# Optimization experiments

Hardware: AMD Instinct MI355X
Metric: run time of the kernel (lower is better)

The kernel has to match this reference:

```python
import jax, jax.numpy as jnp
import numpy as np

B, C, T = 8, 1024, 1024
H, K, R = 8, 8, 8
DQK = C // K      # 128, per-head q/k channels
DFC1 = C // R     # 128, FC hidden
DINNER = C // H   # 128, per-head FC output


def setup_inputs() -> dict:
    key = jax.random.key(0)
    ks = jax.random.split(key, 12)
    s_in = 1.0 / np.sqrt(C)
    s_fc = 1.0 / np.sqrt(DFC1)
    return {
        "x": jax.random.normal(ks[0], (B, C, T), dtype=jnp.float32),
        # per-head 1x1 conv weights stacked over heads
        "Wq": jax.random.normal(ks[1], (H, DQK, C), dtype=jnp.float32) * s_in,
        "bq": jax.random.normal(ks[2], (H, DQK), dtype=jnp.float32) * 0.01,
        "Wk": jax.random.normal(ks[3], (H, DQK, C), dtype=jnp.float32) * s_in,
        "bk": jax.random.normal(ks[4], (H, DQK), dtype=jnp.float32) * 0.01,
        "Wv": jax.random.normal(ks[5], (H, C, C), dtype=jnp.float32) * s_in,
        "bv": jax.random.normal(ks[6], (H, C), dtype=jnp.float32) * 0.01,
        # gamma is zero-init in torch; use small random values to exercise the math
        "gamma": jax.random.normal(ks[7], (H,), dtype=jnp.float32) * 0.1,
        # post-concat MLP (nn.Linear weights, shape (out, in))
        "W1": jax.random.normal(ks[8], (DFC1, C), dtype=jnp.float32) * s_in,
        "b1": jax.random.normal(ks[9], (DFC1,), dtype=jnp.float32) * 0.01,
        "W2": jax.random.normal(ks[10], (DINNER, DFC1), dtype=jnp.float32) * s_fc,
        "b2": jax.random.normal(ks[11], (DINNER,), dtype=jnp.float32) * 0.01,
    }


def reference(x, Wq, bq, Wk, bk, Wv, bv, gamma, W1, b1, W2, b2):
    # x: (B, C, T). 1x1 Conv1d == channel-wise linear; batch all H heads at once.
    q = jnp.einsum('hoc,bct->bhot', Wq, x) + bq[None, :, :, None]  # (B,H,DQK,T)
    k = jnp.einsum('hoc,bct->bhot', Wk, x) + bk[None, :, :, None]  # (B,H,DQK,T)
    v = jnp.einsum('hoc,bct->bhot', Wv, x) + bv[None, :, :, None]  # (B,H,C,T)
    # energy[b,h,t,s] = q[:, :, :, t] . k[:, :, :, s]; softmax over s (no scaling, as in source)
    attn = jax.nn.softmax(jnp.einsum('bhot,bhos->bhts', q, k), axis=-1)  # (B,H,T,T)
    # out[b,h,c,t] = sum_s v[b,h,c,s] * attn[b,h,t,s]
    o = jnp.einsum('bhcs,bhts->bhct', v, attn)                     # (B,H,C,T)
    heads = gamma[None, :, None, None] * o + x[:, None, :, :]      # (B,H,C,T)
    # torch.stack(outs, 2): (B, C, H, T)
    out = heads.transpose(0, 2, 1, 3).reshape(B, C, H * T)
    out = out.transpose(0, 2, 1)                                   # (B, H*T, C)
    # fcs: Linear -> ReLU -> Dropout(eval: identity) -> Linear -> ReLU -> Dropout
    out = jax.nn.relu(out @ W1.T + b1)
    out = jax.nn.relu(out @ W2.T + b2)                             # (B, H*T, DINNER)
    out = out.transpose(0, 2, 1).reshape(B, DINNER * H, T)         # (B, C, T)
    return out + x
```

## Files before the change

kernel.cpp:

```cpp
#include <hip/hip_runtime.h>
#include <hip/hip_bf16.h>

typedef __hip_bfloat16 bf16;
typedef __attribute__((ext_vector_type(8))) __bf16 bf16x8;
typedef __attribute__((ext_vector_type(4))) float f32x4;

typedef const __attribute__((address_space(1))) void gvoid;
typedef __attribute__((address_space(3))) void lvoid;

template<int MODE, int QKLAY>
__global__ __launch_bounds__(256, 2)
void gemm256(const bf16* __restrict__ A, long lda, long sAb, long sAh,
             const bf16* __restrict__ B, long ldb, long sBb, long sBh,
             void* __restrict__ Cv, long ldc, long sCb, long sCh,
             int K,
             const float* __restrict__ bias, long sBiasZ,
             const float* __restrict__ gamma,
             const bf16* __restrict__ xt, long ldxt)
{
    __shared__ bf16 ring[3][(256 + 128) * 32];
    const int nt4 = QKLAY ? blockIdx.x : (blockIdx.x >> 3);
    const int zh  = QKLAY ? 0 : (blockIdx.x & 7);
    const int zb  = QKLAY ? 0 : blockIdx.z;
    const bf16* Ab = A + (long)zb * sAb + (long)zh * sAh + (long)blockIdx.y * 256 * lda;
    const bf16* Bb = B + (long)zb * sBb + (long)zh * sBh + (long)nt4 * 128 * ldb;
    const int tid = threadIdx.x;
    const int wave = tid >> 6, lane = tid & 63;
    const int col = lane & 15, quad = lane >> 4;
    const int wm = wave * 64;

    const bf16* aAddr[4];
    const bf16* bAddr[2];
    int aDst[4], bDst[2];
    #pragma unroll
    for (int i = 0; i < 4; ++i) {
        int cbase = i * 256 + wave * 64;
        int c = cbase + lane;
        int p = c >> 3;
        int sp = (c & 7) ^ (p & 7);
        int m = 2 * p + (sp >> 2);
        int j = sp & 3;
        aAddr[i] = Ab + (long)m * lda + (j << 3);
        aDst[i] = cbase * 8;
    }
    #pragma unroll
    for (int i = 0; i < 2; ++i) {
        int cbase = i * 256 + wave * 64;
        int c = cbase + lane;
        int p = c >> 3;
        int sp = (c & 7) ^ (p & 7);
        int m = 2 * p + (sp >> 2);
        int j = sp & 3;
        bAddr[i] = Bb + (long)m * ldb + (j << 3);
        bDst[i] = 8192 + cbase * 8;
    }

    int offA[4], offB[8];
    #pragma unroll
    for (int mi = 0; mi < 4; ++mi) {
        int m = wm + mi * 16 + col;
        int p = m >> 1;
        int s = (quad | ((m & 1) << 2)) ^ (p & 7);
        offA[mi] = p * 64 + s * 8;
    }
    #pragma unroll
    for (int ni = 0; ni < 8; ++ni) {
        int n = ni * 16 + col;
        int pn = n >> 1;
        int sn = (quad | ((n & 1) << 2)) ^ (pn & 7);
        offB[ni] = 8192 + pn * 64 + sn * 8;
    }

    f32x4 acc[4][8] = {};

    auto STAGE = [&](int rb) {
        bf16* base = &ring[rb][0];
        #pragma unroll
        for (int i = 0; i < 4; ++i) {
            __builtin_amdgcn_global_load_lds((gvoid*)aAddr[i], (lvoid*)(base + aDst[i]), 16, 0, 0);
            aAddr[i] += 32;
        }
        #pragma unroll
        for (int i = 0; i < 2; ++i) {
            __builtin_amdgcn_global_load_lds((gvoid*)bAddr[i], (lvoid*)(base + bDst[i]), 16, 0, 0);
            bAddr[i] += 32;
        }
    };

    const int NT = K >> 5;
    STAGE(0);
    STAGE(1);
    asm volatile("s_waitcnt vmcnt(6)" ::: "memory");
    __builtin_amdgcn_s_barrier();
    __builtin_amdgcn_sched_barrier(0);

    int rc = 0;
    for (int t = 0; t < NT; ++t) {
        int r2 = rc + 2; if (r2 >= 3) r2 -= 3;
        if (t + 2 < NT) STAGE(r2);
        const bf16* buf = &ring[rc][0];
        bf16x8 af[4], bfr[8];
        #pragma unroll
        for (int mi = 0; mi < 4; ++mi)
            af[mi] = *(const bf16x8*)(buf + offA[mi]);
        #pragma unroll
        for (int ni = 0; ni < 8; ++ni)
            bfr[ni] = *(const bf16x8*)(buf + offB[ni]);
        #pragma unroll
        for (int mi = 0; mi < 4; ++mi)
            #pragma unroll
            for (int ni = 0; ni < 8; ++ni)
                acc[mi][ni] = __builtin_amdgcn_mfma_f32_16x16x32_bf16(
                    af[mi], bfr[ni], acc[mi][ni], 0, 0, 0);
        if (t + 2 < NT)
            asm volatile("s_waitcnt vmcnt(6)" ::: "memory");
        else if (t + 1 < NT)
            asm volatile("s_waitcnt vmcnt(0)" ::: "memory");
        if (t + 1 < NT) {
            __builtin_amdgcn_s_barrier();
            __builtin_amdgcn_sched_barrier(0);
        }
        rc = rc + 1; if (rc >= 3) rc -= 3;
    }

    const long m0 = (long)blockIdx.y * 256 + wm;
    const long n0 = (long)nt4 * 128;
    float g = 0.f;
    if (MODE == 3) g = gamma[zh];
    float bn[8];
    if constexpr (MODE == 1) {
        #pragma unroll
        for (int ni = 0; ni < 8; ++ni)
            bn[ni] = bias[n0 + ni * 16 + col];
    }
    #pragma unroll
    for (int mi = 0; mi < 4; ++mi) {
        #pragma unroll
        for (int ni = 0; ni < 8; ++ni) {
            long mb = m0 + mi * 16 + quad * 4;
            long n  = n0 + ni * 16 + col;
            if constexpr (MODE == 0) {
                bf16* cp = (bf16*)Cv + (long)zb * sCb + (long)zh * sCh + mb * ldc + n;
                const float* bp = bias + zh * sBiasZ + mb;
                #pragma unroll
                for (int r = 0; r < 4; ++r) {
                    *cp = __float2bfloat16(acc[mi][ni][r] + bp[r]);
                    cp += ldc;
                }
            } else if constexpr (MODE == 1) {
                bf16* cp = (bf16*)Cv + mb * ldc + n;
                #pragma unroll
                for (int r = 0; r < 4; ++r) {
                    *cp = __float2bfloat16(acc[mi][ni][r] + bn[ni]);
                    cp += ldc;
                }
            } else {
                bf16* cp = (bf16*)Cv + (long)zb * sCb + (long)zh * sCh + mb * ldc + n;
                const bf16* xp = xt + (long)zb * 1048576 + mb * ldxt + n;
                #pragma unroll
                for (int r = 0; r < 4; ++r) {
                    float xv = __bfloat162float(*xp);
                    *cp = __float2bfloat16(g * acc[mi][ni][r] + xv);
                    cp += ldc;
                    xp += ldxt;
                }
            }
        }
    }
}

__global__ __launch_bounds__(256, 2)
void fc_fused(const bf16* __restrict__ ot,
              const bf16* __restrict__ W1b,
              const bf16* __restrict__ W2b,
              const float* __restrict__ b1,
              const float* __restrict__ b2,
              float* __restrict__ outp,
              const float* __restrict__ xf)
{
    __shared__ bf16 As[128 * 64];
    __shared__ bf16 Bs[128 * 64];
    __shared__ bf16 y1[128 * 128];
    const int tid = threadIdx.x;
    const int wave = tid >> 6, lane = tid & 63;
    const int col = lane & 15, quad = lane >> 4;
    const int wm = (wave & 1) * 64, wn = (wave >> 1) * 64;
    const bf16* Ab = ot + (long)blockIdx.y * 128 * 1024;

    const bf16* aAddr[4];
    const bf16* bAddr[4];
    #pragma unroll
    for (int i = 0; i < 4; ++i) {
        int cbase = i * 256 + wave * 64;
        int c = cbase + lane;
        int m = c >> 3, j = c & 7;
        int kch = ((j ^ (m & 7)) << 3);
        aAddr[i] = Ab + (long)m * 1024 + kch;
        bAddr[i] = W1b + (long)m * 1024 + kch;
    }
    int offA[2][4], offB[2][4];
    #pragma unroll
    for (int x = 0; x < 2; ++x) {
        int kq = x * 4 + quad;
        #pragma unroll
        for (int mi = 0; mi < 4; ++mi) {
            int m = wm + mi * 16 + col;
            offA[x][mi] = m * 64 + ((kq ^ (m & 7)) << 3);
            int n = wn + mi * 16 + col;
            offB[x][mi] = n * 64 + ((kq ^ (n & 7)) << 3);
        }
    }

    f32x4 acc[4][4] = {};
    for (int k0 = 0; k0 < 1024; k0 += 64) {
        __syncthreads();
        #pragma unroll
        for (int i = 0; i < 4; ++i) {
            int cbase = i * 256 + wave * 64;
            __builtin_amdgcn_global_load_lds(
                (gvoid*)aAddr[i], (lvoid*)(As + cbase * 8), 16, 0, 0);
            __builtin_amdgcn_global_load_lds(
                (gvoid*)bAddr[i], (lvoid*)(Bs + cbase * 8), 16, 0, 0);
            aAddr[i] += 64;
            bAddr[i] += 64;
        }
        __syncthreads();
        #pragma unroll
        for (int x = 0; x < 2; ++x) {
            bf16x8 af[4], bfr[4];
            #pragma unroll
            for (int mi = 0; mi < 4; ++mi)
                af[mi] = *(const bf16x8*)(As + offA[x][mi]);
            #pragma unroll
            for (int ni = 0; ni < 4; ++ni)
                bfr[ni] = *(const bf16x8*)(Bs + offB[x][ni]);
            #pragma unroll
            for (int mi = 0; mi < 4; ++mi)
                #pragma unroll
                for (int ni = 0; ni < 4; ++ni)
                    acc[mi][ni] = __builtin_amdgcn_mfma_f32_16x16x32_bf16(
                        af[mi], bfr[ni], acc[mi][ni], 0, 0, 0);
        }
    }

    float bn1[4];
    #pragma unroll
    for (int ni = 0; ni < 4; ++ni) bn1[ni] = b1[wn + ni * 16 + col];
    #pragma unroll
    for (int mi = 0; mi < 4; ++mi) {
        #pragma unroll
        for (int ni = 0; ni < 4; ++ni) {
            int mb = wm + mi * 16 + quad * 4;
            int n  = wn + ni * 16 + col;
            int nc = n >> 3, nr = n & 7;
            #pragma unroll
            for (int r = 0; r < 4; ++r) {
                float v = acc[mi][ni][r] + bn1[ni];
                v = v > 0.f ? v : 0.f;
                int m = mb + r;
                y1[m * 128 + (((nc) ^ (m & 7)) << 3) + nr] = __float2bfloat16(v);
            }
        }
    }
    __syncthreads();

    f32x4 acc2[4][4] = {};
    #pragma unroll
    for (int kk = 0; kk < 4; ++kk) {
        int kq = kk * 4 + quad;
        bf16x8 af2[4], bf2[4];
        #pragma unroll
        for (int mi = 0; mi < 4; ++mi) {
            int m = wm + mi * 16 + col;
            af2[mi] = *(const bf16x8*)(y1 + m * 128 + ((kq ^ (m & 7)) << 3));
        }
        #pragma unroll
        for (int ni = 0; ni < 4; ++ni) {
            int n = wn + ni * 16 + col;
            bf2[ni] = *(const bf16x8*)(W2b + n * 128 + kq * 8);
        }
        #pragma unroll
        for (int mi = 0; mi < 4; ++mi)
            #pragma unroll
            for (int ni = 0; ni < 4; ++ni)
                acc2[mi][ni] = __builtin_amdgcn_mfma_f32_16x16x32_bf16(
                    af2[mi], bf2[ni], acc2[mi][ni], 0, 0, 0);
    }

    float bn2[4];
    #pragma unroll
    for (int ni = 0; ni < 4; ++ni) bn2[ni] = b2[wn + ni * 16 + col];
    const long m0 = (long)blockIdx.y * 128 + wm;
    #pragma unroll
    for (int mi = 0; mi < 4; ++mi) {
        #pragma unroll
        for (int ni = 0; ni < 4; ++ni) {
            long mb = m0 + mi * 16 + quad * 4;
            long n  = wn + ni * 16 + col;
            #pragma unroll
            for (int r = 0; r < 4; ++r) {
                long m = mb + r;
                float v = acc2[mi][ni][r] + bn2[ni];
                v = v > 0.f ? v : 0.f;
                long bb = m >> 13, h = (m >> 10) & 7, t = m & 1023;
                long oi = bb * 1048576 + (n * 8 + h) * 1024 + t;
                outp[oi] = v + xf[oi];
            }
        }
    }
}

__global__ __launch_bounds__(256, 2)
void attn_fused(const bf16* __restrict__ qk, bf16* __restrict__ attn)
{
    constexpr int PAD = 1032;
    __shared__ __align__(16) char smraw[73728];
    __shared__ float red[2][4][32];
    bf16* Qs = (bf16*)smraw;
    bf16* Sbuf = (bf16*)smraw;

    const int z = blockIdx.x;
    const int zb = z >> 3, zh = z & 7;
    const int t0 = blockIdx.y * 32;
    const int tid = threadIdx.x, w = tid >> 6, lane = tid & 63;
    const int col = lane & 15, quad = lane >> 4;

    const bf16* Qbase = qk + ((long)zb * 1024 + t0) * 2048 + zh * 256;
    const bf16* Kbase = qk + (long)zb * 1024 * 2048 + zh * 256 + 128;

    auto stageK = [&](int slot, int si) {
        bf16* Ks = (bf16*)(smraw + 8192 + slot * 32768);
        const bf16* Kb = Kbase + (long)si * 128 * 2048;
        #pragma unroll
        for (int i = 0; i < 8; ++i) {
            int cbase = i * 256 + w * 64;
            int c = cbase + lane;
            int m = c >> 4, j = c & 15;
            __builtin_amdgcn_global_load_lds(
                (gvoid*)(Kb + (long)m * 2048 + ((j ^ (m & 7)) << 3)),
                (lvoid*)(Ks + cbase * 8), 16, 0, 0);
        }
    };

    #pragma unroll
    for (int i = 0; i < 2; ++i) {
        int cbase = i * 256 + w * 64;
        int c = cbase + lane;
        int m = c >> 4, j = c & 15;
        __builtin_amdgcn_global_load_lds(
            (gvoid*)(Qbase + (long)m * 2048 + ((j ^ (m & 7)) << 3)),
            (lvoid*)(Qs + cbase * 8), 16, 0, 0);
    }
    stageK(0, 0);
    stageK(1, 1);
    asm volatile("s_waitcnt vmcnt(8)" ::: "memory");
    __builtin_amdgcn_s_barrier();
    __builtin_amdgcn_sched_barrier(0);

    bf16x8 af[2][4];
    #pragma unroll
    for (int mi = 0; mi < 2; ++mi) {
        int m = mi * 16 + col;
        #pragma unroll
        for (int ki = 0; ki < 4; ++ki)
            af[mi][ki] = *(const bf16x8*)(Qs + m * 128 + ((((ki << 2) + quad) ^ (m & 7)) << 3));
    }

    f32x4 acc[2][16] = {};
    #pragma unroll
    for (int si = 0; si < 8; ++si) {
        const bf16* Ks = (const bf16*)(smraw + 8192 + (si & 1) * 32768);
        bf16x8 bfr[2][4];
        #pragma unroll
        for (int ni = 0; ni < 2; ++ni) {
            int n = w * 32 + ni * 16 + col;
            #pragma unroll
            for (int ki = 0; ki < 4; ++ki)
                bfr[ni][ki] = *(const bf16x8*)(Ks + n * 128 + ((((ki << 2) + quad) ^ (n & 7)) << 3));
        }
        asm volatile("s_waitcnt lgkmcnt(0)" ::: "memory");
        __builtin_amdgcn_sched_barrier(0);
        #pragma unroll
        for (int ki = 0; ki < 4; ++ki)
            #pragma unroll
            for (int mi = 0; mi < 2; ++mi)
                #pragma unroll
                for (int ni = 0; ni < 2; ++ni)
                    acc[mi][si * 2 + ni] = __builtin_amdgcn_mfma_f32_16x16x32_bf16(
                        af[mi][ki], bfr[ni][ki], acc[mi][si * 2 + ni], 0, 0, 0);
        __builtin_amdgcn_s_barrier();
        if (si + 2 < 8) {
            stageK(si & 1, si + 2);
            asm volatile("s_waitcnt vmcnt(8)" ::: "memory");
        } else {
            asm volatile("s_waitcnt vmcnt(0)" ::: "memory");
        }
        __builtin_amdgcn_s_barrier();
        __builtin_amdgcn_sched_barrier(0);
    }

    float rmx[2][4], rinv[2][4];
    #pragma unroll
    for (int mi = 0; mi < 2; ++mi)
        #pragma unroll
        for (int r = 0; r < 4; ++r) {
            float mx = acc[mi][0][r];
            #pragma unroll
            for (int j = 1; j < 16; ++j) mx = fmaxf(mx, acc[mi][j][r]);
            #pragma unroll
            for (int off = 1; off < 16; off <<= 1) mx = fmaxf(mx, __shfl_xor(mx, off, 64));
            rmx[mi][r] = mx;
        }
    if (col == 0) {
        #pragma unroll
        for (int mi = 0; mi < 2; ++mi)
            #pragma unroll
            for (int r = 0; r < 4; ++r)
                red[0][w][mi * 16 + quad * 4 + r] = rmx[mi][r];
    }
    __syncthreads();
    #pragma unroll
    for (int mi = 0; mi < 2; ++mi)
        #pragma unroll
        for (int r = 0; r < 4; ++r) {
            int row = mi * 16 + quad * 4 + r;
            rmx[mi][r] = fmaxf(fmaxf(red[0][0][row], red[0][1][row]),
                               fmaxf(red[0][2][row], red[0][3][row]));
        }
    #pragma unroll
    for (int mi = 0; mi < 2; ++mi)
        #pragma unroll
        for (int r = 0; r < 4; ++r) {
            float s = 0.f;
            #pragma unroll
            for (int j = 0; j < 16; ++j) {
                acc[mi][j][r] = __expf(acc[mi][j][r] - rmx[mi][r]);
                s += acc[mi][j][r];
            }
            #pragma unroll
            for (int off = 1; off < 16; off <<= 1) s += __shfl_xor(s, off, 64);
            rinv[mi][r] = s;
        }
    if (col == 0) {
        #pragma unroll
        for (int mi = 0; mi < 2; ++mi)
            #pragma unroll
            for (int r = 0; r < 4; ++r)
                red[1][w][mi * 16 + quad * 4 + r] = rinv[mi][r];
    }
    __syncthreads();
    #pragma unroll
    for (int mi = 0; mi < 2; ++mi)
        #pragma unroll
        for (int r = 0; r < 4; ++r) {
            int row = mi * 16 + quad * 4 + r;
            float s4 = red[1][0][row] + red[1][1][row] + red[1][2][row] + red[1][3][row];
            rinv[mi][r] = 1.0f / s4;
        }

    bf16* dst = attn + ((long)(zb * 8 + zh)) * 1048576 + (long)t0 * 1024;
    #pragma unroll
    for (int mi = 0; mi < 2; ++mi) {
        __syncthreads();
        #pragma unroll
        for (int j = 0; j < 16; ++j) {
            int colb = (j >> 1) * 128 + w * 32 + (j & 1) * 16 + col;
            #pragma unroll
            for (int r = 0; r < 4; ++r) {
                int rowh = quad * 4 + r;
                Sbuf[rowh * PAD + colb] = __float2bfloat16(acc[mi][j][r] * rinv[mi][r]);
            }
        }
        __syncthreads();
        #pragma unroll
        for (int i = 0; i < 8; ++i) {
            int c = i * 256 + tid;
            int rowh = c >> 7, jj = c & 127;
            bf16x8 vv = *(const bf16x8*)(Sbuf + rowh * PAD + jj * 8);
            *(bf16x8*)(dst + (long)(mi * 16 + rowh) * 1024 + jj * 8) = vv;
        }
    }
}

__global__ __launch_bounds__(256)
void transpose_cast_x(const float* __restrict__ x, bf16* __restrict__ xt)
{
    __shared__ float tile[32][33];
    int b = blockIdx.z;
    int c0 = blockIdx.y * 32, t0 = blockIdx.x * 32;
    int tx = threadIdx.x & 31, ty = threadIdx.x >> 5;
    const float* xb = x + (long)b * 1024 * 1024;
    #pragma unroll
    for (int i = 0; i < 4; ++i) {
        int c = ty + i * 8;
        tile[c][tx] = xb[(long)(c0 + c) * 1024 + t0 + tx];
    }
    __syncthreads();
    bf16* xtb = xt + (long)b * 1024 * 1024;
    #pragma unroll
    for (int i = 0; i < 4; ++i) {
        int t = ty + i * 8;
        xtb[(long)(t0 + t) * 1024 + c0 + tx] = __float2bfloat16(tile[tx][t]);
    }
}

__global__ __launch_bounds__(256)
void cast_f2b(const float* __restrict__ in, bf16* __restrict__ out, long n)
{
    long i = (long)blockIdx.x * 256 + threadIdx.x;
    long stride = (long)gridDim.x * 256;
    for (; i < n; i += stride) out[i] = __float2bfloat16(in[i]);
}

__global__ __launch_bounds__(256)
void build_wqk(const float* __restrict__ Wq, const float* __restrict__ Wk,
               const float* __restrict__ bq, const float* __restrict__ bk,
               bf16* __restrict__ Wqk, float* __restrict__ biasqk)
{
    long i = (long)blockIdx.x * 256 + threadIdx.x;
    long r = i >> 10, c = i & 1023;
    long h = r >> 8, rr = r & 255;
    float v = (rr < 128) ? Wq[(h * 128 + rr) * 1024 + c]
                         : Wk[(h * 128 + (rr - 128)) * 1024 + c];
    Wqk[i] = __float2bfloat16(v);
    if (c == 0)
        biasqk[r] = (rr < 128) ? bq[h * 128 + rr] : bk[h * 128 + rr - 128];
}

extern "C" void kernel_launch(void* const* d_in, const int* in_sizes, int n_in,
                              void* d_out, int out_size, void* d_ws, size_t ws_size,
                              hipStream_t stream)
{
    const float* x     = (const float*)d_in[0];
    const float* Wq    = (const float*)d_in[1];
    const float* bq    = (const float*)d_in[2];
    const float* Wk    = (const float*)d_in[3];
    const float* bk    = (const float*)d_in[4];
    const float* Wv    = (const float*)d_in[5];
    const float* bv    = (const float*)d_in[6];
    const float* gamma = (const float*)d_in[7];
    const float* W1    = (const float*)d_in[8];
    const float* b1    = (const float*)d_in[9];
    const float* W2    = (const float*)d_in[10];
    const float* b2    = (const float*)d_in[11];
    float* out = (float*)d_out;

    char* base = (char*)d_ws;
    const long MB = 1048576;
    bf16*  xt   = (bf16*)(base);
    bf16*  Wvb  = (bf16*)(base + 16 * MB);
    bf16*  vbuf = (bf16*)(base + 32 * MB);
    bf16*  Wqk  = (bf16*)(base + 32 * MB);
    float* bqk  = (float*)(base + 36 * MB);
    bf16*  attb = (bf16*)(base + 96 * MB);
    bf16*  W1b  = (bf16*)(base + 96 * MB);
    bf16*  W2b  = (bf16*)(base + 96 * MB + 524288);
    bf16*  ot   = (bf16*)(base + 160 * MB);
    bf16*  qkt  = (bf16*)(base + 224 * MB);

    dim3 blk(256);
    transpose_cast_x<<<dim3(32, 32, 8), blk, 0, stream>>>(x, xt);
    build_wqk<<<8192, blk, 0, stream>>>(Wq, Wk, bq, bk, Wqk, bqk);
    cast_f2b<<<4096, blk, 0, stream>>>(Wv, Wvb, 8192ll * 1024);

    const long M1 = 1048576, M2 = 2097152, M8 = 8388608;

    gemm256<1, 1><<<dim3(16, 32, 1), blk, 0, stream>>>(
        xt, 1024, 0, 0, Wqk, 1024, 0, 0, qkt, 2048, 0, 0, 1024,
        bqk, 0, nullptr, nullptr, 0);

    for (int q = 0; q < 2; ++q) {
        const long b0 = (long)q * 4;
        const bf16* xtq = xt + b0 * M1;
        gemm256<0, 0><<<dim3(64, 4, 4), blk, 0, stream>>>(
            Wvb, 1024, 0, M1, xtq, 1024, M1, 0, vbuf, 1024, M8, M1, 1024,
            bv, 1024, nullptr, nullptr, 0);
        attn_fused<<<dim3(32, 32, 1), blk, 0, stream>>>(
            qkt + b0 * M2, attb);
        gemm256<3, 0><<<dim3(64, 4, 4), blk, 0, stream>>>(
            attb, 1024, M8, M1, vbuf, 1024, M8, M1,
            ot, 1024, M8, M1, 1024,
            nullptr, 0, gamma, xtq, 1024);
        cast_f2b<<<512, blk, 0, stream>>>(W1, W1b, 128 * 1024);
        cast_f2b<<<64, blk, 0, stream>>>(W2, W2b, 128 * 128);
        fc_fused<<<dim3(1, 256, 1), blk, 0, stream>>>(
            ot, W1b, W2b, b1, b2, out + b0 * M1, x + b0 * M1);
    }
}
```

Measured before the change: 645.1 us.

## Pipeline FC1 K-loop with three-stage LDS ring of 32-wide tiles

The first GEMM in the fused FC kernel used to load a 64-wide K tile, synchronize, then compute, so global loads never overlapped with MFMA work. It now uses a three-buffer LDS ring of 32-wide K tiles, prefetching two stages ahead with vmcnt-based waits and a single barrier per iteration. The swizzle packs two rows per 64-element line to keep reads bank-conflict free. This doubles the iteration count and adds barrier overhead, and it relies on the vmcnt counts being correct.

```diff
diff --git a/kernel.cpp b/kernel.cpp
--- a/kernel.cpp
+++ b/kernel.cpp
@@ -178,8 +178,7 @@
               float* __restrict__ outp,
               const float* __restrict__ xf)
 {
-    __shared__ bf16 As[128 * 64];
-    __shared__ bf16 Bs[128 * 64];
+    __shared__ bf16 ring[3][128 * 32 * 2];
     __shared__ bf16 y1[128 * 128];
     const int tid = threadIdx.x;
     const int wave = tid >> 6, lane = tid & 63;
@@ -187,60 +186,85 @@
     const int wm = (wave & 1) * 64, wn = (wave >> 1) * 64;
     const bf16* Ab = ot + (long)blockIdx.y * 128 * 1024;
 
-    const bf16* aAddr[4];
-    const bf16* bAddr[4];
-    #pragma unroll
-    for (int i = 0; i < 4; ++i) {
+    const bf16* aAddr[2];
+    const bf16* bAddr[2];
+    int aDst[2], bDst[2];
+    #pragma unroll
+    for (int i = 0; i < 2; ++i) {
         int cbase = i * 256 + wave * 64;
         int c = cbase + lane;
-        int m = c >> 3, j = c & 7;
-        int kch = ((j ^ (m & 7)) << 3);
-        aAddr[i] = Ab + (long)m * 1024 + kch;
-        bAddr[i] = W1b + (long)m * 1024 + kch;
-    }
-    int offA[2][4], offB[2][4];
-    #pragma unroll
-    for (int x = 0; x < 2; ++x) {
-        int kq = x * 4 + quad;
-        #pragma unroll
-        for (int mi = 0; mi < 4; ++mi) {
-            int m = wm + mi * 16 + col;
-            offA[x][mi] = m * 64 + ((kq ^ (m & 7)) << 3);
-            int n = wn + mi * 16 + col;
-            offB[x][mi] = n * 64 + ((kq ^ (n & 7)) << 3);
-        }
-    }
+        int p = c >> 3;
+        int sp = (c & 7) ^ (p & 7);
+        int m = 2 * p + (sp >> 2);
+        int j = sp & 3;
+        aAddr[i] = Ab + (long)m * 1024 + (j << 3);
+        aDst[i] = cbase * 8;
+        bAddr[i] = W1b + (long)m * 1024 + (j << 3);
+        bDst[i] = 4096 + cbase * 8;
+    }
+
+    int offA[4], offB[4];
+    #pragma unroll
+    for (int mi = 0; mi < 4; ++mi) {
+        int m = wm + mi * 16 + col;
+        int p = m >> 1;
+        int s = (quad | ((m & 1) << 2)) ^ (p & 7);
+        offA[mi] = p * 64 + s * 8;
+        int n = wn + mi * 16 + col;
+        int pn = n >> 1;
+        int sn = (quad | ((n & 1) << 2)) ^ (pn & 7);
+        offB[mi] = 4096 + pn * 64 + sn * 8;
+    }
+
+    auto STAGE = [&](int rb) {
+        bf16* base = &ring[rb][0];
+        #pragma unroll
+        for (int i = 0; i < 2; ++i) {
+            __builtin_amdgcn_global_load_lds((gvoid*)aAddr[i], (lvoid*)(base + aDst[i]), 16, 0, 0);
+            aAddr[i] += 32;
+        }
+        #pragma unroll
+        for (int i = 0; i < 2; ++i) {
+            __builtin_amdgcn_global_load_lds((gvoid*)bAddr[i], (lvoid*)(base + bDst[i]), 16, 0, 0);
+            bAddr[i] += 32;
+        }
+    };
 
     f32x4 acc[4][4] = {};
-    for (int k0 = 0; k0 < 1024; k0 += 64) {
-        __syncthreads();
-        #pragma unroll
-        for (int i = 0; i < 4; ++i) {
-            int cbase = i * 256 + wave * 64;
-            __builtin_amdgcn_global_load_lds(
-                (gvoid*)aAddr[i], (lvoid*)(As + cbase * 8), 16, 0, 0);
-            __builtin_amdgcn_global_load_lds(
-                (gvoid*)bAddr[i], (lvoid*)(Bs + cbase * 8), 16, 0, 0);
-            aAddr[i] += 64;
-            bAddr[i] += 64;
-        }
-        __syncthreads();
-        #pragma unroll
-        for (int x = 0; x < 2; ++x) {
-            bf16x8 af[4], bfr[4];
-            #pragma unroll
-            for (int mi = 0; mi < 4; ++mi)
-                af[mi] = *(const bf16x8*)(As + offA[x][mi]);
+    const int NT = 32;
+    STAGE(0);
+    STAGE(1);
+    asm volatile("s_waitcnt vmcnt(4)" ::: "memory");
+    __builtin_amdgcn_s_barrier();
+    __builtin_amdgcn_sched_barrier(0);
+
+    int rc = 0;
+    for (int t = 0; t < NT; ++t) {
+        int r2 = rc + 2; if (r2 >= 3) r2 -= 3;
+        if (t + 2 < NT) STAGE(r2);
+        const bf16* buf = &ring[rc][0];
+        bf16x8 af[4], bfr[4];
+        #pragma unroll
+        for (int mi = 0; mi < 4; ++mi)
+            af[mi] = *(const bf16x8*)(buf + offA[mi]);
+        #pragma unroll
+        for (int ni = 0; ni < 4; ++ni)
+            bfr[ni] = *(const bf16x8*)(buf + offB[ni]);
+        #pragma unroll
+        for (int mi = 0; mi < 4; ++mi)
             #pragma unroll
             for (int ni = 0; ni < 4; ++ni)
-                bfr[ni] = *(const bf16x8*)(Bs + offB[x][ni]);
-            #pragma unroll
-            for (int mi = 0; mi < 4; ++mi)
-                #pragma unroll
-                for (int ni = 0; ni < 4; ++ni)
-                    acc[mi][ni] = __builtin_amdgcn_mfma_f32_16x16x32_bf16(
-                        af[mi], bfr[ni], acc[mi][ni], 0, 0, 0);
-        }
+                acc[mi][ni] = __builtin_amdgcn_mfma_f32_16x16x32_bf16(
+                    af[mi], bfr[ni], acc[mi][ni], 0, 0, 0);
+        if (t + 2 < NT)
+            asm volatile("s_waitcnt vmcnt(4)" ::: "memory");
+        else if (t + 1 < NT)
+            asm volatile("s_waitcnt vmcnt(0)" ::: "memory");
+        if (t + 1 < NT) {
+            __builtin_amdgcn_s_barrier();
+            __builtin_amdgcn_sched_barrier(0);
+        }
+        rc = rc + 1; if (rc >= 3) rc -= 3;
     }
 
     float bn1[4];
```

Measured after the change: 643.3 us. About the same (-0.3%).
